# Optimization experiments

Hardware: AMD Instinct MI355X
Metric: run time of the kernel (lower is better)

Reference implementation:

```python
import jax, jax.numpy as jnp
import numpy as np


def setup_inputs() -> dict:
    key = jax.random.key(0)
    k1, k2 = jax.random.split(key)
    x = jax.random.normal(k1, (1, 48, 56, 56), dtype=jnp.float32)
    w = jax.random.normal(k2, (24, 96, 7), dtype=jnp.float32)
    return {"x": x, "w": w, "shift": 1}


def reference(x, w, shift):
    # The torch unfold + einsum is a grouped cross-correlation along W:
    #   x viewed as (1, groups=2, Cin=24, H=56, W=56)
    #   out[l,o,k,n,m] = sum_{i,j} x[l,o,i,n, m+j-3] * w[i,k,j]   (zero-padded)
    # Same weight w is shared by both groups -> duplicate it per group.
    wt = jnp.transpose(w, (1, 0, 2))               # (96, 24, 7)  OIK per group
    kernel = jnp.concatenate([wt, wt], axis=0)     # (192, 24, 7) both groups
    kernel = kernel[:, :, None, :]                 # (O=192, I=24, KH=1, KW=7)
    y = jax.lax.conv_general_dilated(
        x, kernel,
        window_strides=(1, 1),
        padding=((0, 0), (3, 3)),                  # 'same' along W only
        dimension_numbers=("NCHW", "OIHW", "NCHW"),
        feature_group_count=2,
    )                                              # (1, 192, 56, 56)
    # torch.roll(t, shift, dims=2): roll along H
    return jnp.roll(y, shift, axis=2)
```

## Files before the change

### kernel.cpp

```cpp
#include <hip/hip_runtime.h>


#define H 56
#define W 56
#define C_GRP 24
#define KW 7
#define HW (H * W)

__global__ __launch_bounds__(64) void conv7_roll_kernel(
    const float* __restrict__ x,
    const float* __restrict__ w,
    const int* __restrict__ shift_p,
    float* __restrict__ out)
{
    const int o     = blockIdx.x;
    const int htile = blockIdx.y;
    const int lane  = threadIdx.x;
    const int r     = lane >> 3;
    const int s     = lane & 7;
    const int h_out = htile * 8 + r;
    const int wbase = s * 7;

    const int g  = o / 96;
    const int oc = o % 96;

    __shared__ float wl[C_GRP * KW];
    for (int t = lane; t < C_GRP * KW; t += 64) {
        const int i = t / 7;
        const int k = t - i * 7;
        wl[t] = w[i * (96 * 7) + oc * 7 + k];
    }
    __syncthreads();

    const int shift = shift_p[0];
    int hi = (h_out - shift) % H;
    if (hi < 0) hi += H;

    float acc[7] = {0.f, 0.f, 0.f, 0.f, 0.f, 0.f, 0.f};

    const float* xg = x + (g * C_GRP) * HW + hi * W;

    for (int i = 0; i < C_GRP; ++i) {
        const float* xr = xg + i * HW;
        float xv[13];
        #pragma unroll
        for (int j = 0; j < 13; ++j) {
            const int p = wbase - 3 + j;
            xv[j] = (p >= 0 && p < W) ? xr[p] : 0.0f;
        }
        #pragma unroll
        for (int k = 0; k < KW; ++k) {
            const float wk = wl[i * KW + k];
            #pragma unroll
            for (int j = 0; j < 7; ++j)
                acc[j] += xv[j + k] * wk;
        }
    }

    float* op = out + o * HW + h_out * W + wbase;
    #pragma unroll
    for (int j = 0; j < 7; ++j)
        op[j] = acc[j];
}

extern "C" void kernel_launch(void* const* d_in, const int* in_sizes, int n_in,
                              void* d_out, int out_size, void* d_ws, size_t ws_size,
                              hipStream_t stream)
{
    const float* x     = (const float*)d_in[0];
    const float* w     = (const float*)d_in[1];
    const int*   shift = (const int*)d_in[2];
    float*       out   = (float*)d_out;

    dim3 grid(192, 7);
    conv7_roll_kernel<<<grid, 64, 0, stream>>>(x, w, shift, out);
}
```

Before: 71.82 us.

## Stage rolled input rows in padded LDS tile shared by four output channels

Each 256-thread block now loads the 24-channel, 8-row input slab once into shared memory with float4 loads and zero-padded halos, so the four wavefronts (one output channel each) reuse it. Bounds checks in the inner loop go away. Weights are read through a wave-uniform pointer built with readfirstlane, which lets them become scalar loads instead of going through LDS. This trades more LDS per block (about 52KB), and therefore lower occupancy, for a large cut in redundant global input reads.

```diff
diff --git a/kernel.cpp b/kernel.cpp
--- a/kernel.cpp
+++ b/kernel.cpp
@@ -1,63 +1,76 @@
 #include <hip/hip_runtime.h>
 
 
-#define H 56
-#define W 56
-#define C_GRP 24
-#define KW 7
-#define HW (H * W)
+#define H   56
+#define W   56
+#define CG  24
+#define KW  7
+#define HW_ (H * W)
+#define STR 68
+#define COFF 4
 
-__global__ __launch_bounds__(64) void conv7_roll_kernel(
+__global__ __launch_bounds__(256) void conv7_roll_kernel(
     const float* __restrict__ x,
     const float* __restrict__ w,
     const int* __restrict__ shift_p,
     float* __restrict__ out)
 {
-    const int o     = blockIdx.x;
-    const int htile = blockIdx.y;
-    const int lane  = threadIdx.x;
-    const int r     = lane >> 3;
-    const int s     = lane & 7;
-    const int h_out = htile * 8 + r;
-    const int wbase = s * 7;
+    const int g     = blockIdx.x;
+    const int ocq   = blockIdx.y;
+    const int htile = blockIdx.z;
+    const int tid   = threadIdx.x;
 
-    const int g  = o / 96;
-    const int oc = o % 96;
+    __shared__ float xs[CG * 8 * STR];
 
-    __shared__ float wl[C_GRP * KW];
-    for (int t = lane; t < C_GRP * KW; t += 64) {
-        const int i = t / 7;
-        const int k = t - i * 7;
-        wl[t] = w[i * (96 * 7) + oc * 7 + k];
+    const int shift = shift_p[0];
+    const int h0    = htile * 8;
+
+    const float* xg = x + g * CG * HW_;
+    for (int t = tid; t < CG * 8 * 14; t += 256) {
+        const int ch = t / 112;
+        const int rq = t - ch * 112;
+        const int r  = rq / 14;
+        const int q  = rq - r * 14;
+        int hi = (h0 + r - shift) % H; if (hi < 0) hi += H;
+        const float4 v = *(const float4*)(xg + ch * HW_ + hi * W + q * 4);
+        *(float4*)(&xs[(ch * 8 + r) * STR + COFF + q * 4]) = v;
+    }
+    for (int t = tid; t < CG * 8 * 3; t += 256) {
+        const int row   = t / 3;
+        const int which = t - row * 3;
+        const int col   = (which == 0) ? 0 : (which == 1 ? 60 : 64);
+        *(float4*)(&xs[row * STR + col]) = make_float4(0.f, 0.f, 0.f, 0.f);
     }
     __syncthreads();
 
-    const int shift = shift_p[0];
-    int hi = (h_out - shift) % H;
-    if (hi < 0) hi += H;
+    const int wv   = tid >> 6;
+    const int lane = tid & 63;
+    const int r    = lane >> 3;
+    const int s    = lane & 7;
+    const int oc   = __builtin_amdgcn_readfirstlane(ocq * 4 + wv);
+    const float* wp = w + oc * KW;
 
     float acc[7] = {0.f, 0.f, 0.f, 0.f, 0.f, 0.f, 0.f};
 
-    const float* xg = x + (g * C_GRP) * HW + hi * W;
+    const float* xrow = &xs[r * STR + 7 * s + 1];
 
-    for (int i = 0; i < C_GRP; ++i) {
-        const float* xr = xg + i * HW;
+    #pragma unroll 4
+    for (int i = 0; i < CG; ++i) {
+        const float* xr = xrow + i * (8 * STR);
         float xv[13];
         #pragma unroll
-        for (int j = 0; j < 13; ++j) {
-            const int p = wbase - 3 + j;
-            xv[j] = (p >= 0 && p < W) ? xr[p] : 0.0f;
-        }
+        for (int j = 0; j < 13; ++j) xv[j] = xr[j];
         #pragma unroll
         for (int k = 0; k < KW; ++k) {
-            const float wk = wl[i * KW + k];
+            const float wk = wp[i * (96 * KW) + k];
             #pragma unroll
             for (int j = 0; j < 7; ++j)
                 acc[j] += xv[j + k] * wk;
         }
     }
 
-    float* op = out + o * HW + h_out * W + wbase;
+    const int h_out = h0 + r;
+    float* op = out + (g * 96 + oc) * HW_ + h_out * W + 7 * s;
     #pragma unroll
     for (int j = 0; j < 7; ++j)
         op[j] = acc[j];
@@ -72,6 +85,6 @@
     const int*   shift = (const int*)d_in[2];
     float*       out   = (float*)d_out;
 
-    dim3 grid(192, 7);
-    conv7_roll_kernel<<<grid, 64, 0, stream>>>(x, w, shift, out);
+    dim3 grid(2, 24, 7);
+    conv7_roll_kernel<<<grid, 256, 0, stream>>>(x, w, shift, out);
 }
```

New measurement: 72.04 us. No clear change (+0.3%).
